# Performance work log

Hardware: AMD Instinct MI355X
Metric: run time of the kernel (lower is better)

## Reference

```python
import jax, jax.numpy as jnp
import numpy as np

EMBED_DIM = 1024
NUM_HEADS = 16
HEAD_DIM = EMBED_DIM // NUM_HEADS


def setup_inputs() -> dict:
    key = jax.random.key(0)
    k1, k2, k3, k4, k5 = jax.random.split(key, 5)
    x = jax.random.normal(k1, (4, 2048, EMBED_DIM), dtype=jnp.float32)
    # nn.Linear params: weight [out, in], bias [out]
    s_in = 1.0 / np.sqrt(EMBED_DIM)
    W_qkv = jax.random.uniform(k2, (3 * EMBED_DIM, EMBED_DIM), jnp.float32, -s_in, s_in)
    b_qkv = jax.random.uniform(k3, (3 * EMBED_DIM,), jnp.float32, -s_in, s_in)
    W_out = jax.random.uniform(k4, (EMBED_DIM, EMBED_DIM), jnp.float32, -s_in, s_in)
    b_out = jax.random.uniform(k5, (EMBED_DIM,), jnp.float32, -s_in, s_in)
    return {"x": x, "W_qkv": W_qkv, "b_qkv": b_qkv, "W_out": W_out, "b_out": b_out}


def reference(x, W_qkv, b_qkv, W_out, b_out):
    B, S, D = x.shape
    H, Dh = NUM_HEADS, HEAD_DIM
    qkv = x @ W_qkv.T + b_qkv                      # [B, S, 3D]
    qkv = qkv.reshape(B, S, 3, H, Dh)
    q = qkv[:, :, 0].transpose(0, 2, 1, 3)        # [B, H, S, Dh]
    k = qkv[:, :, 1].transpose(0, 2, 1, 3)
    v = qkv[:, :, 2].transpose(0, 2, 1, 3)
    scale = 1.0 / jnp.sqrt(jnp.asarray(Dh, x.dtype))
    scores = jnp.einsum('bhqd,bhkd->bhqk', q, k) * scale  # [B, H, S, S]
    attn = jax.nn.softmax(scores, axis=-1)
    out = jnp.einsum('bhqk,bhkd->bhqd', attn, v)  # [B, H, S, Dh]
    out = out.transpose(0, 2, 1, 3).reshape(B, S, D)
    return out @ W_out.T + b_out
```

## Files before the change

kernel.cpp:

```cpp
#include <hip/hip_runtime.h>

#define BB 4
#define SS 2048
#define DD 1024
#define HH 16
#define DHH 64
#define MM (BB*SS)

typedef __bf16 bf16x8 __attribute__((ext_vector_type(8)));
typedef __bf16 bf16x4 __attribute__((ext_vector_type(4)));
typedef float  f32x4  __attribute__((ext_vector_type(4)));

__device__ __forceinline__ unsigned short f2bf(float x) {
    unsigned int u = __float_as_uint(x);
    u += 0x7FFFu + ((u >> 16) & 1u);
    return (unsigned short)(u >> 16);
}

__device__ __forceinline__ void glds16(const __bf16* g, __bf16* l) {
    __builtin_amdgcn_global_load_lds(
        (const __attribute__((address_space(1))) void*)g,
        (__attribute__((address_space(3))) void*)l, 16, 0, 0);
}

__global__ __launch_bounds__(256) void cvt_all(
    const float4* __restrict__ x,  const float4* __restrict__ wq,
    const float4* __restrict__ wo,
    ushort4* __restrict__ xb, ushort4* __restrict__ wqb, ushort4* __restrict__ wob)
{
    int i = blockIdx.x * 256 + threadIdx.x;
    const float4* src; ushort4* dst; int j;
    if (i < 2097152)      { src = x;  dst = xb;  j = i; }
    else if (i < 2883584) { src = wq; dst = wqb; j = i - 2097152; }
    else                  { src = wo; dst = wob; j = i - 2883584; }
    float4 v = src[j];
    ushort4 o;
    o.x = f2bf(v.x); o.y = f2bf(v.y); o.z = f2bf(v.z); o.w = f2bf(v.w);
    dst[j] = o;
}

__global__ __launch_bounds__(256) void qkv_gemm(
    const __bf16* __restrict__ A,
    const __bf16* __restrict__ W,
    const float* __restrict__ bias,
    __bf16* __restrict__ Qp,
    __bf16* __restrict__ Kp,
    __bf16* __restrict__ Vp)
{
    __shared__ __bf16 smem[16896];
#define CT(r,c) smem[(r)*132 + (c)]
    __bf16* As = smem;
    __bf16* Bs = smem + 8192;
    const int tid  = threadIdx.x;
    const int m0   = blockIdx.x * 128;
    const int n0   = blockIdx.y * 128;
    const int lane = tid & 63;
    const int wid  = tid >> 6;
    const int fr   = lane & 15;
    const int quad = lane >> 4;
    const int wm   = (wid >> 1) * 64;
    const int wn   = (wid & 1) * 64;

    const int srow = lane >> 3;
    const int sg   = ((lane & 7) - srow) & 7;

    f32x4 acc[4][4] = {};

    for (int k0 = 0; k0 < DD; k0 += 64) {
        __syncthreads();
        #pragma unroll
        for (int p = 0; p < 4; ++p) {
            int cidx = p * 4 + wid;
            int r = cidx * 8 + srow;
            glds16(A + (size_t)(m0 + r) * DD + k0 + sg * 8, As + cidx * 512);
            glds16(W + (size_t)(n0 + r) * DD + k0 + sg * 8, Bs + cidx * 512);
        }
        __syncthreads();

        bf16x8 af[2][4], bw[2][4];
        #pragma unroll
        for (int kc = 0; kc < 2; ++kc)
            #pragma unroll
            for (int t = 0; t < 4; ++t) {
                int col = ((kc * 4 + quad + fr) & 7) * 8;
                af[kc][t] = *(const bf16x8*)&As[(wm + t*16 + fr) * 64 + col];
                bw[kc][t] = *(const bf16x8*)&Bs[(wn + t*16 + fr) * 64 + col];
            }
        #pragma unroll
        for (int kc = 0; kc < 2; ++kc)
            #pragma unroll
            for (int mt = 0; mt < 4; ++mt)
                #pragma unroll
                for (int nt = 0; nt < 4; ++nt)
                    acc[mt][nt] = __builtin_amdgcn_mfma_f32_16x16x32_bf16(
                        af[kc][mt], bw[kc][nt], acc[mt][nt], 0, 0, 0);
    }

    __syncthreads();
    const int t3 = n0 >> 10;
    const int b  = m0 >> 11;
    const int s0 = m0 & (SS - 1);

    float bn[4];
    #pragma unroll
    for (int nt = 0; nt < 4; ++nt) bn[nt] = bias[n0 + wn + nt*16 + fr];

    if (t3 == 2) {
        #pragma unroll
        for (int nt = 0; nt < 4; ++nt)
            #pragma unroll
            for (int mt = 0; mt < 4; ++mt) {
                f32x4 t;
                #pragma unroll
                for (int i = 0; i < 4; ++i) t[i] = acc[mt][nt][i] + bn[nt];
                *(bf16x4*)&CT(wn + nt*16 + fr, wm + mt*16 + quad*4) =
                    __builtin_convertvector(t, bf16x4);
            }
        __syncthreads();
        const int pn0 = n0 - 2048;
        #pragma unroll
        for (int p = 0; p < 8; ++p) {
            int g = tid + p * 256;
            int r = g >> 4;
            int c = (g & 15) << 3;
            int pn = pn0 + r, h = pn >> 6, dh = pn & 63;
            *(uint4*)&Vp[((size_t)((b*HH + h)*DHH + dh))*SS + s0 + c] = *(uint4*)&CT(r, c);
        }
    } else {
        __bf16* dst = (t3 == 0) ? Qp : Kp;
        const float qscale = (t3 == 0) ? 0.125f * 1.44269504088896340736f : 1.0f;
        #pragma unroll
        for (int nt = 0; nt < 4; ++nt)
            #pragma unroll
            for (int mt = 0; mt < 4; ++mt)
                #pragma unroll
                for (int i = 0; i < 4; ++i)
                    CT(wm + mt*16 + quad*4 + i, wn + nt*16 + fr) =
                        (__bf16)((acc[mt][nt][i] + bn[nt]) * qscale);
        __syncthreads();
        const int pn0 = (t3 == 0) ? n0 : n0 - 1024;
        #pragma unroll
        for (int p = 0; p < 8; ++p) {
            int g = tid + p * 256;
            int r = g >> 4;
            int c = (g & 15) << 3;
            int pn = pn0 + c, h = pn >> 6, dh = pn & 63;
            *(uint4*)&dst[((size_t)((b*HH + h))*SS + s0 + r)*DHH + dh] = *(uint4*)&CT(r, c);
        }
    }
#undef CT
}

__global__ __launch_bounds__(256) void out_gemm(
    const __bf16* __restrict__ A,
    const __bf16* __restrict__ W,
    const float* __restrict__ bias,
    float* __restrict__ out)
{
    __shared__ __bf16 smem[16384];
    __bf16* As = smem;
    __bf16* Bs = smem + 8192;
    const int tid  = threadIdx.x;
    const int m0   = blockIdx.x * 128;
    const int n0   = blockIdx.y * 128;
    const int lane = tid & 63;
    const int wid  = tid >> 6;
    const int fr   = lane & 15;
    const int quad = lane >> 4;
    const int wm   = (wid >> 1) * 64;
    const int wn   = (wid & 1) * 64;

    const int srow = lane >> 3;
    const int sg   = ((lane & 7) - srow) & 7;

    f32x4 acc[4][4] = {};

    for (int k0 = 0; k0 < DD; k0 += 64) {
        __syncthreads();
        #pragma unroll
        for (int p = 0; p < 4; ++p) {
            int cidx = p * 4 + wid;
            int r = cidx * 8 + srow;
            glds16(A + (size_t)(m0 + r) * DD + k0 + sg * 8, As + cidx * 512);
            glds16(W + (size_t)(n0 + r) * DD + k0 + sg * 8, Bs + cidx * 512);
        }
        __syncthreads();

        bf16x8 af[2][4], bw[2][4];
        #pragma unroll
        for (int kc = 0; kc < 2; ++kc)
            #pragma unroll
            for (int t = 0; t < 4; ++t) {
                int col = ((kc * 4 + quad + fr) & 7) * 8;
                af[kc][t] = *(const bf16x8*)&As[(wm + t*16 + fr) * 64 + col];
                bw[kc][t] = *(const bf16x8*)&Bs[(wn + t*16 + fr) * 64 + col];
            }
        #pragma unroll
        for (int kc = 0; kc < 2; ++kc)
            #pragma unroll
            for (int mt = 0; mt < 4; ++mt)
                #pragma unroll
                for (int nt = 0; nt < 4; ++nt)
                    acc[mt][nt] = __builtin_amdgcn_mfma_f32_16x16x32_bf16(
                        af[kc][mt], bw[kc][nt], acc[mt][nt], 0, 0, 0);
    }

    #pragma unroll
    for (int nt = 0; nt < 4; ++nt) {
        int n  = n0 + wn + nt*16 + fr;
        float bnv = bias[n];
        #pragma unroll
        for (int mt = 0; mt < 4; ++mt) {
            #pragma unroll
            for (int i = 0; i < 4; ++i) {
                int m = m0 + wm + mt*16 + quad*4 + i;
                out[(size_t)m * DD + n] = acc[mt][nt][i] + bnv;
            }
        }
    }
}

__global__ __launch_bounds__(256, 2) void attn_mfma(
    const __bf16* __restrict__ Qp,
    const __bf16* __restrict__ Kp,
    const __bf16* __restrict__ Vp,
    __bf16* __restrict__ Op)
{
    __shared__ __bf16 Ks[64 * 64];
    __shared__ __bf16 VT[64 * 64];
    __shared__ __bf16 Ps[256][72];
    __shared__ float  Ls[256];

    const int tid  = threadIdx.x;
    const int q0   = blockIdx.x * 256;
    const int bh   = blockIdx.y;
    const size_t base = (size_t)bh * SS * DHH;
    const int lane = tid & 63;
    const int wid  = tid >> 6;
    const int fr   = lane & 15;
    const int quad = lane >> 4;
    const int wrow = wid * 64;

    const int srow = lane >> 3;
    const int sg   = ((lane & 7) - srow) & 7;

    bf16x8 aq[4][2];
    #pragma unroll
    for (int nt = 0; nt < 4; ++nt)
        #pragma unroll
        for (int kc = 0; kc < 2; ++kc)
            aq[nt][kc] = *(const bf16x8*)
                (Qp + base + (size_t)(q0 + wrow + nt*16 + fr) * DHH + kc*32 + quad*8);

    f32x4 o[4][4] = {};
    float lp[4] = {};

    for (int kt = 0; kt < SS; kt += 64) {
        __syncthreads();
        #pragma unroll
        for (int p = 0; p < 2; ++p) {
            int cidx = p * 4 + wid;
            int r = cidx * 8 + srow;
            glds16(Kp + base + (size_t)(kt + r) * DHH + sg * 8, Ks + cidx * 512);
            glds16(Vp + base + (size_t)r * SS + kt + sg * 8, VT + cidx * 512);
        }
        __syncthreads();

        #pragma unroll
        for (int mt = 0; mt < 4; ++mt) {
            bf16x8 bk[2];
            #pragma unroll
            for (int kc = 0; kc < 2; ++kc)
                bk[kc] = *(const bf16x8*)
                    &Ks[(mt*16 + fr) * 64 + ((kc*4 + quad + fr) & 7) * 8];
            f32x4 s[4] = {};
            #pragma unroll
            for (int nt = 0; nt < 4; ++nt)
                #pragma unroll
                for (int kc = 0; kc < 2; ++kc)
                    s[nt] = __builtin_amdgcn_mfma_f32_16x16x32_bf16(
                        bk[kc], aq[nt][kc], s[nt], 0, 0, 0);
            #pragma unroll
            for (int nt = 0; nt < 4; ++nt) {
                f32x4 ev;
                ev[0] = __builtin_amdgcn_exp2f(s[nt][0]);
                ev[1] = __builtin_amdgcn_exp2f(s[nt][1]);
                ev[2] = __builtin_amdgcn_exp2f(s[nt][2]);
                ev[3] = __builtin_amdgcn_exp2f(s[nt][3]);
                lp[nt] += (ev[0] + ev[1]) + (ev[2] + ev[3]);
                *(bf16x4*)&Ps[wrow + nt*16 + fr][mt*16 + quad*4] =
                    __builtin_convertvector(ev, bf16x4);
            }
        }

        #pragma unroll
        for (int mt = 0; mt < 4; ++mt) {
            bf16x8 ap[2];
            #pragma unroll
            for (int kc = 0; kc < 2; ++kc)
                ap[kc] = *(const bf16x8*)&Ps[wrow + mt*16 + fr][kc*32 + quad*8];
            #pragma unroll
            for (int nt = 0; nt < 4; ++nt)
                #pragma unroll
                for (int kc = 0; kc < 2; ++kc) {
                    bf16x8 bv = *(const bf16x8*)
                        &VT[(nt*16 + fr) * 64 + ((kc*4 + quad + fr) & 7) * 8];
                    o[mt][nt] = __builtin_amdgcn_mfma_f32_16x16x32_bf16(
                        ap[kc], bv, o[mt][nt], 0, 0, 0);
                }
        }
    }

    #pragma unroll
    for (int nt = 0; nt < 4; ++nt) {
        float v = lp[nt];
        v += __shfl_xor(v, 16);
        v += __shfl_xor(v, 32);
        Ls[wrow + nt*16 + fr] = v;
    }

    #pragma unroll
    for (int mt = 0; mt < 4; ++mt)
        #pragma unroll
        for (int i = 0; i < 4; ++i) {
            float inv = 1.0f / Ls[wrow + mt*16 + quad*4 + i];
            #pragma unroll
            for (int nt = 0; nt < 4; ++nt)
                Ps[wrow + mt*16 + quad*4 + i][nt*16 + fr] = (__bf16)(o[mt][nt][i] * inv);
        }
    __syncthreads();

    const int b = bh >> 4, h = bh & (HH - 1);
    #pragma unroll
    for (int p = 0; p < 8; ++p) {
        int g = tid + p * 256;
        int r = g >> 3;
        int c = (g & 7) << 3;
        *(uint4*)&Op[((size_t)(b*SS + q0 + r))*DD + h*DHH + c] = *(uint4*)&Ps[r][c];
    }
}


extern "C" void kernel_launch(void* const* d_in, const int* in_sizes, int n_in,
                              void* d_out, int out_size, void* d_ws, size_t ws_size,
                              hipStream_t stream)
{
    const float* x     = (const float*)d_in[0];
    const float* W_qkv = (const float*)d_in[1];
    const float* b_qkv = (const float*)d_in[2];
    const float* W_out = (const float*)d_in[3];
    const float* b_out = (const float*)d_in[4];
    float* out = (float*)d_out;

    __bf16* ws  = (__bf16*)d_ws;
    __bf16* xb  = ws;
    __bf16* wqb = xb  + (size_t)8388608;
    __bf16* wob = wqb + (size_t)3145728;
    __bf16* qp  = wob + (size_t)1048576;
    __bf16* kp  = qp  + (size_t)8388608;
    __bf16* vp  = kp  + (size_t)8388608;
    __bf16* op  = vp  + (size_t)8388608;

    cvt_all<<<12288, 256, 0, stream>>>(
        (const float4*)x, (const float4*)W_qkv, (const float4*)W_out,
        (ushort4*)xb, (ushort4*)wqb, (ushort4*)wob);

    qkv_gemm<<<dim3(MM/128, 3*DD/128), 256, 0, stream>>>(xb, wqb, b_qkv, qp, kp, vp);
    attn_mfma<<<dim3(SS/256, BB*HH), 256, 0, stream>>>(qp, kp, vp, op);
    out_gemm<<<dim3(MM/128, DD/128), 256, 0, stream>>>(op, wob, b_out, out);
}
```

Measured before the change: 266.4 us.

## Double-buffer K/V tiles in attention and raise MFMA wave priority

The attention kernel now keeps two LDS buffers for K and V and issues the async global-to-LDS loads for the next key tile before computing on the current one. This cuts the loop from two barriers per iteration to one and lets the load latency overlap with the MFMA and exp work. It also wraps the MFMA sections in s_setprio so waves in their matrix phase get issue priority. The cost is an extra 16 KB of LDS per block, which could reduce how many blocks fit on a CU, and correctness relies on the barrier waiting for the async LDS loads to finish.

Result: no change. 265.6 us (-0.3%).

```diff
diff --git a/kernel.cpp b/kernel.cpp
--- a/kernel.cpp
+++ b/kernel.cpp
@@ -226,8 +226,8 @@
     const __bf16* __restrict__ Vp,
     __bf16* __restrict__ Op)
 {
-    __shared__ __bf16 Ks[64 * 64];
-    __shared__ __bf16 VT[64 * 64];
+    __shared__ __bf16 Ks[2][64 * 64];
+    __shared__ __bf16 VT[2][64 * 64];
     __shared__ __bf16 Ps[256][72];
     __shared__ float  Ls[256];
 
@@ -244,6 +244,19 @@
     const int srow = lane >> 3;
     const int sg   = ((lane & 7) - srow) & 7;
 
+#define STAGE_KV(buf, kt_)                                                        \
+    {                                                                             \
+        _Pragma("unroll")                                                         \
+        for (int p = 0; p < 2; ++p) {                                             \
+            int cidx = p * 4 + wid;                  \
+            int r = cidx * 8 + srow;                                              \
+            glds16(Kp + base + (size_t)((kt_) + r) * DHH + sg * 8,                \
+                   &Ks[buf][cidx * 512]);                                         \
+            glds16(Vp + base + (size_t)r * SS + (kt_) + sg * 8,                   \
+                   &VT[buf][cidx * 512]);                                         \
+        }                                                                         \
+    }
+
     bf16x8 aq[4][2];
     #pragma unroll
     for (int nt = 0; nt < 4; ++nt)
@@ -255,16 +268,14 @@
     f32x4 o[4][4] = {};
     float lp[4] = {};
 
+    STAGE_KV(0, 0)
+    __syncthreads();
+
+    int cur = 0;
     for (int kt = 0; kt < SS; kt += 64) {
-        __syncthreads();
-        #pragma unroll
-        for (int p = 0; p < 2; ++p) {
-            int cidx = p * 4 + wid;
-            int r = cidx * 8 + srow;
-            glds16(Kp + base + (size_t)(kt + r) * DHH + sg * 8, Ks + cidx * 512);
-            glds16(Vp + base + (size_t)r * SS + kt + sg * 8, VT + cidx * 512);
-        }
-        __syncthreads();
+        if (kt + 64 < SS) STAGE_KV(cur ^ 1, kt + 64)
+        const __bf16* Kc = Ks[cur];
+        const __bf16* Vc = VT[cur];
 
         #pragma unroll
         for (int mt = 0; mt < 4; ++mt) {
@@ -272,14 +283,16 @@
             #pragma unroll
             for (int kc = 0; kc < 2; ++kc)
                 bk[kc] = *(const bf16x8*)
-                    &Ks[(mt*16 + fr) * 64 + ((kc*4 + quad + fr) & 7) * 8];
+                    &Kc[(mt*16 + fr) * 64 + ((kc*4 + quad + fr) & 7) * 8];
             f32x4 s[4] = {};
+            __builtin_amdgcn_s_setprio(1);
             #pragma unroll
             for (int nt = 0; nt < 4; ++nt)
                 #pragma unroll
                 for (int kc = 0; kc < 2; ++kc)
                     s[nt] = __builtin_amdgcn_mfma_f32_16x16x32_bf16(
                         bk[kc], aq[nt][kc], s[nt], 0, 0, 0);
+            __builtin_amdgcn_s_setprio(0);
             #pragma unroll
             for (int nt = 0; nt < 4; ++nt) {
                 f32x4 ev;
@@ -299,17 +312,23 @@
             #pragma unroll
             for (int kc = 0; kc < 2; ++kc)
                 ap[kc] = *(const bf16x8*)&Ps[wrow + mt*16 + fr][kc*32 + quad*8];
+            __builtin_amdgcn_s_setprio(1);
             #pragma unroll
             for (int nt = 0; nt < 4; ++nt)
                 #pragma unroll
                 for (int kc = 0; kc < 2; ++kc) {
                     bf16x8 bv = *(const bf16x8*)
-                        &VT[(nt*16 + fr) * 64 + ((kc*4 + quad + fr) & 7) * 8];
+                        &Vc[(nt*16 + fr) * 64 + ((kc*4 + quad + fr) & 7) * 8];
                     o[mt][nt] = __builtin_amdgcn_mfma_f32_16x16x32_bf16(
                         ap[kc], bv, o[mt][nt], 0, 0, 0);
                 }
-        }
-    }
+            __builtin_amdgcn_s_setprio(0);
+        }
+
+        __syncthreads();
+        cur ^= 1;
+    }
+#undef STAGE_KV
 
     #pragma unroll
     for (int nt = 0; nt < 4; ++nt) {
```
